# Kernel optimization log

Measured on AMD Instinct MI355X. Metric: run time of the kernel, lower is better.

## Reference

```python
import jax, jax.numpy as jnp
import numpy as np

N_NODES = 100000
N_EDGES = 1600000
IN_CH = 128
HID = 128
N_GRAPHS = 512
N_CLASSES = 64
BN_EPS = 1e-5


def setup_inputs() -> dict:
    key = jax.random.key(0)
    ks = jax.random.split(key, 16)
    x = jax.random.normal(ks[0], (N_NODES, IN_CH), dtype=jnp.float32)
    edge_index = jax.random.randint(ks[1], (2, N_EDGES), 0, N_NODES, dtype=jnp.int32)
    batch = jnp.sort(jax.random.randint(ks[2], (N_NODES,), 0, N_GRAPHS, dtype=jnp.int32))
    def lin(k, fan_in, fan_out):
        s = 1.0 / np.sqrt(fan_in)
        kw, kb = jax.random.split(k)
        W = jax.random.uniform(kw, (fan_in, fan_out), minval=-s, maxval=s, dtype=jnp.float32)
        b = jax.random.uniform(kb, (fan_out,), minval=-s, maxval=s, dtype=jnp.float32)
        return W, b
    W1, b1 = lin(ks[3], IN_CH, HID)
    W2, b2 = lin(ks[4], HID, HID)
    W3, b3 = lin(ks[5], HID, HID)
    Wh, bh = lin(ks[6], HID * 3, N_CLASSES)
    ones = jnp.ones((HID,), jnp.float32)
    zeros = jnp.zeros((HID,), jnp.float32)
    return {
        'x': x, 'edge_index': edge_index, 'batch': batch,
        'W1': W1, 'b1': b1, 'g1': ones, 'be1': zeros,
        'W2': W2, 'b2': b2, 'g2': ones, 'be2': zeros,
        'W3': W3, 'b3': b3, 'g3': ones, 'be3': zeros,
        'Wh': Wh, 'bh': bh,
    }


def _gcn_conv(x, W, b, src, dst, dinv):
    # PyG GCNConv: h = x @ W; out_i = sum_{j->i} dinv_j*dinv_i*h_j + dinv_i^2*h_i (self-loop) + b
    h = x @ W
    coef = (dinv[src] * dinv[dst])[:, None]           # [E,1]
    msg = coef * h[src]                                # [E,H] gather
    agg = jax.ops.segment_sum(msg, dst, num_segments=x.shape[0])  # scatter-add
    return agg + h * (dinv * dinv)[:, None] + b


def _bn(x, g, b):
    mu = jnp.mean(x, axis=0)
    var = jnp.mean((x - mu) ** 2, axis=0)  # biased var (torch training BN)
    return (x - mu) * jax.lax.rsqrt(var + BN_EPS) * g + b


def reference(x, edge_index, batch, W1, b1, g1, be1, W2, b2, g2, be2, W3, b3, g3, be3, Wh, bh):
    src, dst = edge_index[0], edge_index[1]
    n = x.shape[0]
    # degree with self-loops, computed over target nodes (PyG gcn_norm default)
    deg = jax.ops.segment_sum(jnp.ones((src.shape[0],), x.dtype), dst, num_segments=n) + 1.0
    dinv = jax.lax.rsqrt(deg)

    h = jax.nn.relu(_bn(_gcn_conv(x, W1, b1, src, dst, dinv), g1, be1))
    h = jax.nn.relu(_bn(_gcn_conv(h, W2, b2, src, dst, dinv), g2, be2) + h)
    h = jax.nn.relu(_bn(_gcn_conv(h, W3, b3, src, dst, dinv), g3, be3) + h)

    # global mean / add / max pooling per graph
    cnt = jax.ops.segment_sum(jnp.ones((n,), h.dtype), batch, num_segments=N_GRAPHS)
    s = jax.ops.segment_sum(h, batch, num_segments=N_GRAPHS)
    mean = s / jnp.maximum(cnt, 1.0)[:, None]
    mx = jax.ops.segment_max(h, batch, num_segments=N_GRAPHS)
    mx = jnp.where(cnt[:, None] > 0, mx, 0.0)
    pooled = jnp.concatenate([mean, s, mx], axis=1)  # [G, 3H]

    # dropout is identity in eval; single output head
    out = pooled @ Wh + bh
    return out
```

## Files before the change

### kernel.cpp

```cpp
#include <hip/hip_runtime.h>
#include <hip/hip_bf16.h>

#define N_NODES   100000
#define N_EDGES   1600000
#define CH        128
#define N_GRAPHS  512
#define BN_EPS    1e-5f
#define N_PAD     100128

typedef unsigned int uint;
typedef unsigned short ushort_t;

typedef short bf16x8 __attribute__((ext_vector_type(8)));
typedef float f32x4  __attribute__((ext_vector_type(4)));

__device__ __forceinline__ ushort_t f2bf(float f) {
    uint u = __float_as_uint(f);
    uint r = (u + 0x7fffu + ((u >> 16) & 1u)) >> 16;
    return (ushort_t)r;
}
__device__ __forceinline__ float bf2f(ushort_t u) {
    return __uint_as_float(((uint)u) << 16);
}
__device__ __forceinline__ float bf2f_lo(uint u) {
    return __uint_as_float(u << 16);
}
__device__ __forceinline__ float bf2f_hi(uint u) {
    return __uint_as_float(u & 0xffff0000u);
}

#define PREP_W_BLOCKS 128
#define GEMM1_BLOCKS  ((N_NODES + 127) / 128)
#define WLDS_PITCH 136

__global__ __launch_bounds__(256) void k_prep(const int* __restrict__ dst,
                                              int* __restrict__ cnt,
                                              int* __restrict__ rank,
                                              const float* __restrict__ W1,
                                              const float* __restrict__ W2,
                                              const float* __restrict__ W3,
                                              ushort_t* __restrict__ Wt,
                                              const float* __restrict__ x,
                                              ushort_t* __restrict__ H) {
    __shared__ ushort_t lws[128 * WLDS_PITCH];
    const int bid = blockIdx.x;

    if (bid < PREP_W_BLOCKS) {
        int tid = bid * 256 + threadIdx.x;
        int l = tid >> 14;
        int e = tid & 16383;
        int n = e >> 7;
        int k = e & 127;
        const float* W = l ? W3 : W2;
        Wt[l * 16384 + n * 128 + k] = f2bf(W[k * 128 + n]);
        return;
    }

    if (bid < PREP_W_BLOCKS + GEMM1_BLOCKS) {
        const int blk = bid - PREP_W_BLOCKS;
        for (int it = 0; it < 64; ++it) {
            int e = it * 256 + threadIdx.x;
            int k = e >> 7;
            int n = e & 127;
            lws[n * WLDS_PITCH + k] = f2bf(W1[e]);
        }
        __syncthreads();

        const int t = threadIdx.x;
        const int wave = t >> 6;
        const int lane = t & 63;
        const int q = lane >> 4;
        const int r = lane & 15;
        const int row0 = blk * 128 + wave * 32;

        bf16x8 afrag[4][2];
#pragma unroll
        for (int i = 0; i < 2; ++i) {
            int rr = row0 + i * 16 + r;
            if (rr > N_NODES - 1) rr = N_NODES - 1;
            const float* rowp = x + (size_t)rr * 128;
#pragma unroll
            for (int ks = 0; ks < 4; ++ks) {
                const int k0 = ks * 32 + q * 8;
                float4 v0 = *(const float4*)(rowp + k0);
                float4 v1 = *(const float4*)(rowp + k0 + 4);
                bf16x8 av;
                av[0] = (short)f2bf(v0.x); av[1] = (short)f2bf(v0.y);
                av[2] = (short)f2bf(v0.z); av[3] = (short)f2bf(v0.w);
                av[4] = (short)f2bf(v1.x); av[5] = (short)f2bf(v1.y);
                av[6] = (short)f2bf(v1.z); av[7] = (short)f2bf(v1.w);
                afrag[ks][i] = av;
            }
        }

        f32x4 acc[2][8];
#pragma unroll
        for (int i = 0; i < 2; ++i)
#pragma unroll
            for (int j = 0; j < 8; ++j)
                acc[i][j] = (f32x4){0.f, 0.f, 0.f, 0.f};

#pragma unroll
        for (int ks = 0; ks < 4; ++ks) {
            const int k0 = ks * 32 + q * 8;
            bf16x8 b[8];
#pragma unroll
            for (int j = 0; j < 8; ++j)
                b[j] = *(const bf16x8*)&lws[(j * 16 + r) * WLDS_PITCH + k0];
#pragma unroll
            for (int i = 0; i < 2; ++i)
#pragma unroll
                for (int j = 0; j < 8; ++j)
                    acc[i][j] = __builtin_amdgcn_mfma_f32_16x16x32_bf16(afrag[ks][i], b[j], acc[i][j], 0, 0, 0);
        }

#pragma unroll
        for (int i = 0; i < 2; ++i) {
#pragma unroll
            for (int rg = 0; rg < 4; ++rg) {
                int rr = row0 + i * 16 + q * 4 + rg;
                if (rr < N_NODES) {
#pragma unroll
                    for (int j = 0; j < 8; ++j)
                        H[(size_t)rr * 128 + j * 16 + r] = f2bf(acc[i][j][rg]);
                }
            }
        }
        return;
    }

    int e = (bid - PREP_W_BLOCKS - GEMM1_BLOCKS) * 256 + threadIdx.x;
    if (e < N_EDGES) rank[e] = atomicAdd(&cnt[dst[e]], 1);
}

__global__ __launch_bounds__(512) void k_scan1(const int* __restrict__ cnt,
                                               int* __restrict__ lofs,
                                               int* __restrict__ bsum) {
    __shared__ int sd[512];
    int t = threadIdx.x;
    int i = blockIdx.x * 512 + t;
    int v = (i < N_NODES) ? cnt[i] : 0;
    sd[t] = v;
    __syncthreads();
    for (int o = 1; o < 512; o <<= 1) {
        int x = (t >= o) ? sd[t - o] : 0;
        __syncthreads();
        sd[t] += x;
        __syncthreads();
    }
    if (i < N_NODES) lofs[i] = sd[t] - v;
    if (t == 511) bsum[blockIdx.x] = sd[511];
}

__global__ __launch_bounds__(256) void k_scan3(const int* __restrict__ lofs,
                                               const int* __restrict__ bsum,
                                               const int* __restrict__ cnt,
                                               int* __restrict__ offs,
                                               float* __restrict__ dinv,
                                               int nblocks) {
    __shared__ int sd[256];
    int t = threadIdx.x;
    int v = (t < nblocks) ? bsum[t] : 0;
    sd[t] = v;
    __syncthreads();
    for (int o = 1; o < 256; o <<= 1) {
        int x = (t >= o) ? sd[t - o] : 0;
        __syncthreads();
        sd[t] += x;
        __syncthreads();
    }
    int exc = sd[t] - v;
    __syncthreads();
    sd[t] = exc;
    __syncthreads();

    int i = blockIdx.x * 256 + t;
    if (i < N_NODES) {
        offs[i] = lofs[i] + sd[i >> 9];
        dinv[i] = rsqrtf((float)cnt[i] + 1.0f);
    }
    if (i == 0) offs[N_NODES] = N_EDGES;
}

__global__ __launch_bounds__(256) void k_fill(const int* __restrict__ src,
                                              const int* __restrict__ dst,
                                              const int* __restrict__ offs,
                                              const int* __restrict__ rank,
                                              int* __restrict__ csr_src) {
    int e = blockIdx.x * 256 + threadIdx.x;
    if (e >= N_EDGES) return;
    int pos = offs[dst[e]] + rank[e];
    csr_src[pos] = src[e];
}

template<int MODE>
__global__ __launch_bounds__(256) void k_gemm(const ushort_t* __restrict__ Ain,
                                              const ushort_t* __restrict__ Wt,
                                              const float* __restrict__ dinv,
                                              ushort_t* __restrict__ H,
                                              const float* __restrict__ stats,
                                              const float* __restrict__ gamma,
                                              const float* __restrict__ beta,
                                              const ushort_t* __restrict__ RES,
                                              ushort_t* __restrict__ XOUT) {
    const int t = threadIdx.x;
    const int wave = t >> 6;
    const int lane = t & 63;
    const int q = lane >> 4;
    const int r = lane & 15;
    const int row0 = blockIdx.x * 128 + wave * 32;

    bf16x8 afrag[4][2];
    const float invN = 1.0f / (float)N_NODES;

#pragma unroll
    for (int ks = 0; ks < 4; ++ks) {
        const int k0 = ks * 32 + q * 8;
        float sc[8], sh[8];
        {
            float4 sm0 = *(const float4*)&stats[k0];
            float4 sm1 = *(const float4*)&stats[k0 + 4];
            float4 sq0 = *(const float4*)&stats[128 + k0];
            float4 sq1 = *(const float4*)&stats[128 + k0 + 4];
            float4 gm0 = *(const float4*)&gamma[k0];
            float4 gm1 = *(const float4*)&gamma[k0 + 4];
            float4 bt0 = *(const float4*)&beta[k0];
            float4 bt1 = *(const float4*)&beta[k0 + 4];
            float sm[8] = {sm0.x, sm0.y, sm0.z, sm0.w, sm1.x, sm1.y, sm1.z, sm1.w};
            float sq[8] = {sq0.x, sq0.y, sq0.z, sq0.w, sq1.x, sq1.y, sq1.z, sq1.w};
            float gm[8] = {gm0.x, gm0.y, gm0.z, gm0.w, gm1.x, gm1.y, gm1.z, gm1.w};
            float bt[8] = {bt0.x, bt0.y, bt0.z, bt0.w, bt1.x, bt1.y, bt1.z, bt1.w};
#pragma unroll
            for (int u = 0; u < 8; ++u) {
                float mu = sm[u] * invN;
                float s  = gm[u] * rsqrtf(sq[u] * invN - mu * mu + BN_EPS);
                sc[u] = s;
                sh[u] = bt[u] - mu * s;
            }
        }
#pragma unroll
        for (int i = 0; i < 2; ++i) {
            int row = row0 + i * 16 + r;
            int rrc = (row < N_NODES) ? row : (N_NODES - 1);
            uint4 av = *(const uint4*)(Ain + (size_t)rrc * 128 + k0);
            float y[8];
            y[0] = bf2f_lo(av.x); y[1] = bf2f_hi(av.x);
            y[2] = bf2f_lo(av.y); y[3] = bf2f_hi(av.y);
            y[4] = bf2f_lo(av.z); y[5] = bf2f_hi(av.z);
            y[6] = bf2f_lo(av.w); y[7] = bf2f_hi(av.w);
#pragma unroll
            for (int u = 0; u < 8; ++u) y[u] = y[u] * sc[u] + sh[u];
            if constexpr (MODE == 3) {
                uint4 rv = *(const uint4*)(RES + (size_t)rrc * 128 + k0);
                y[0] += bf2f_lo(rv.x); y[1] += bf2f_hi(rv.x);
                y[2] += bf2f_lo(rv.y); y[3] += bf2f_hi(rv.y);
                y[4] += bf2f_lo(rv.z); y[5] += bf2f_hi(rv.z);
                y[6] += bf2f_lo(rv.w); y[7] += bf2f_hi(rv.w);
            }
            uint4 o;
            o.x = (uint)f2bf(fmaxf(y[0], 0.f)) | ((uint)f2bf(fmaxf(y[1], 0.f)) << 16);
            o.y = (uint)f2bf(fmaxf(y[2], 0.f)) | ((uint)f2bf(fmaxf(y[3], 0.f)) << 16);
            o.z = (uint)f2bf(fmaxf(y[4], 0.f)) | ((uint)f2bf(fmaxf(y[5], 0.f)) << 16);
            o.w = (uint)f2bf(fmaxf(y[6], 0.f)) | ((uint)f2bf(fmaxf(y[7], 0.f)) << 16);
            afrag[ks][i] = __builtin_bit_cast(bf16x8, o);
            if (row < N_NODES)
                *(uint4*)(XOUT + (size_t)row * 128 + k0) = o;
        }
    }

    f32x4 acc[2][8];
#pragma unroll
    for (int i = 0; i < 2; ++i)
#pragma unroll
        for (int j = 0; j < 8; ++j)
            acc[i][j] = (f32x4){0.f, 0.f, 0.f, 0.f};

#pragma unroll
    for (int ks = 0; ks < 4; ++ks) {
        const int k0 = ks * 32 + q * 8;
        bf16x8 b[8];
#pragma unroll
        for (int j = 0; j < 8; ++j)
            b[j] = *(const bf16x8*)(Wt + (size_t)(j * 16 + r) * 128 + k0);
#pragma unroll
        for (int i = 0; i < 2; ++i)
#pragma unroll
            for (int j = 0; j < 8; ++j)
                acc[i][j] = __builtin_amdgcn_mfma_f32_16x16x32_bf16(afrag[ks][i], b[j], acc[i][j], 0, 0, 0);
    }

#pragma unroll
    for (int i = 0; i < 2; ++i) {
#pragma unroll
        for (int rg = 0; rg < 4; ++rg) {
            int rr = row0 + i * 16 + q * 4 + rg;
            if (rr < N_NODES) {
                float dv = dinv[rr];
#pragma unroll
                for (int j = 0; j < 8; ++j)
                    H[(size_t)rr * 128 + j * 16 + r] = f2bf(acc[i][j][rg] * dv);
            }
        }
    }
}

template<bool PRESCALED>
__global__ __launch_bounds__(256) void k_gather(const int* __restrict__ csr_src,
                                                const int* __restrict__ offs,
                                                const float* __restrict__ dinv,
                                                const ushort_t* __restrict__ H,
                                                const float* __restrict__ b,
                                                ushort_t* __restrict__ AGG) {
    int node = blockIdx.x * 4 + (threadIdx.x >> 6);
    if (node >= N_NODES) return;
    int lane = threadIdx.x & 63;
    int g = lane >> 4;
    int cl = lane & 15;
    int c = cl * 8;

    float a0 = 0.f, a1 = 0.f, a2 = 0.f, a3 = 0.f;
    float a4 = 0.f, a5 = 0.f, a6 = 0.f, a7 = 0.f;
    float dvn = dinv[node];

#define ACC8(hv)  do { \
        a0 += bf2f_lo((hv).x); a1 += bf2f_hi((hv).x); \
        a2 += bf2f_lo((hv).y); a3 += bf2f_hi((hv).y); \
        a4 += bf2f_lo((hv).z); a5 += bf2f_hi((hv).z); \
        a6 += bf2f_lo((hv).w); a7 += bf2f_hi((hv).w); } while (0)
#define ACC8F(hv, dv)  do { \
        a0 = fmaf((dv), bf2f_lo((hv).x), a0); a1 = fmaf((dv), bf2f_hi((hv).x), a1); \
        a2 = fmaf((dv), bf2f_lo((hv).y), a2); a3 = fmaf((dv), bf2f_hi((hv).y), a3); \
        a4 = fmaf((dv), bf2f_lo((hv).z), a4); a5 = fmaf((dv), bf2f_hi((hv).z), a5); \
        a6 = fmaf((dv), bf2f_lo((hv).w), a6); a7 = fmaf((dv), bf2f_hi((hv).w), a7); } while (0)

    if (g == 0) {
        uint4 hv = *(const uint4*)(H + (size_t)node * 128 + c);
        if constexpr (PRESCALED) { ACC8(hv); } else { ACC8F(hv, dvn); }
    }

    int p = offs[node];
    int end = offs[node + 1];

    for (; p + 16 <= end; p += 16) {
        int s0 = csr_src[p      + g], s1 = csr_src[p +  4 + g];
        int s2 = csr_src[p +  8 + g], s3 = csr_src[p + 12 + g];
        uint4 h0 = *(const uint4*)(H + (size_t)s0 * 128 + c);
        uint4 h1 = *(const uint4*)(H + (size_t)s1 * 128 + c);
        uint4 h2 = *(const uint4*)(H + (size_t)s2 * 128 + c);
        uint4 h3 = *(const uint4*)(H + (size_t)s3 * 128 + c);
        if constexpr (PRESCALED) {
            ACC8(h0); ACC8(h1); ACC8(h2); ACC8(h3);
        } else {
            float d0 = dinv[s0], d1 = dinv[s1], d2 = dinv[s2], d3 = dinv[s3];
            ACC8F(h0, d0); ACC8F(h1, d1); ACC8F(h2, d2); ACC8F(h3, d3);
        }
    }
    for (; p + 4 <= end; p += 4) {
        int s0 = csr_src[p + g];
        uint4 h0 = *(const uint4*)(H + (size_t)s0 * 128 + c);
        if constexpr (PRESCALED) { ACC8(h0); }
        else { float d0 = dinv[s0]; ACC8F(h0, d0); }
    }
    if (p < end) {
        int idx = p + g;
        bool ok = idx < end;
        int s0 = csr_src[ok ? idx : p];
        uint4 h0 = *(const uint4*)(H + (size_t)s0 * 128 + c);
        if constexpr (PRESCALED) { if (ok) ACC8(h0); }
        else { float d0 = dinv[s0]; if (ok) ACC8F(h0, d0); }
    }
#undef ACC8
#undef ACC8F

    a0 += __shfl_xor(a0, 16); a1 += __shfl_xor(a1, 16);
    a2 += __shfl_xor(a2, 16); a3 += __shfl_xor(a3, 16);
    a4 += __shfl_xor(a4, 16); a5 += __shfl_xor(a5, 16);
    a6 += __shfl_xor(a6, 16); a7 += __shfl_xor(a7, 16);
    a0 += __shfl_xor(a0, 32); a1 += __shfl_xor(a1, 32);
    a2 += __shfl_xor(a2, 32); a3 += __shfl_xor(a3, 32);
    a4 += __shfl_xor(a4, 32); a5 += __shfl_xor(a5, 32);
    a6 += __shfl_xor(a6, 32); a7 += __shfl_xor(a7, 32);

    if (g == 0) {
        float4 bv0 = *(const float4*)&b[c];
        float4 bv1 = *(const float4*)&b[c + 4];
        a0 = a0 * dvn + bv0.x; a1 = a1 * dvn + bv0.y;
        a2 = a2 * dvn + bv0.z; a3 = a3 * dvn + bv0.w;
        a4 = a4 * dvn + bv1.x; a5 = a5 * dvn + bv1.y;
        a6 = a6 * dvn + bv1.z; a7 = a7 * dvn + bv1.w;
        uint4 o;
        o.x = (uint)f2bf(a0) | ((uint)f2bf(a1) << 16);
        o.y = (uint)f2bf(a2) | ((uint)f2bf(a3) << 16);
        o.z = (uint)f2bf(a4) | ((uint)f2bf(a5) << 16);
        o.w = (uint)f2bf(a6) | ((uint)f2bf(a7) << 16);
        *(uint4*)(AGG + (size_t)node * 128 + c) = o;
    }
}

__global__ __launch_bounds__(512) void k_bn_stats(const ushort_t* __restrict__ AGG,
                                                  float* __restrict__ stats) {
    __shared__ float red[2][16][128];
    int c4 = (threadIdx.x & 31) * 4;
    int rl = threadIdx.x >> 5;
    float s0 = 0.f, s1 = 0.f, s2 = 0.f, s3 = 0.f;
    float q0 = 0.f, q1 = 0.f, q2 = 0.f, q3 = 0.f;
    for (int i = blockIdx.x * 16 + rl; i < N_NODES; i += gridDim.x * 16) {
        uint2 av = *(const uint2*)&AGG[(size_t)i * 128 + c4];
        float v0 = bf2f_lo(av.x), v1 = bf2f_hi(av.x);
        float v2 = bf2f_lo(av.y), v3 = bf2f_hi(av.y);
        s0 += v0; q0 += v0 * v0;
        s1 += v1; q1 += v1 * v1;
        s2 += v2; q2 += v2 * v2;
        s3 += v3; q3 += v3 * v3;
    }
    red[0][rl][c4 + 0] = s0; red[0][rl][c4 + 1] = s1;
    red[0][rl][c4 + 2] = s2; red[0][rl][c4 + 3] = s3;
    red[1][rl][c4 + 0] = q0; red[1][rl][c4 + 1] = q1;
    red[1][rl][c4 + 2] = q2; red[1][rl][c4 + 3] = q3;
    __syncthreads();
    int t = threadIdx.x;
    if (t < 128) {
        float S = 0.f;
#pragma unroll
        for (int k = 0; k < 16; ++k) S += red[0][k][t];
        atomicAdd(&stats[t], S);
    } else if (t < 256) {
        int c = t - 128;
        float Q = 0.f;
#pragma unroll
        for (int k = 0; k < 16; ++k) Q += red[1][k][c];
        atomicAdd(&stats[128 + c], Q);
    }
}

__global__ __launch_bounds__(512) void k_pool(const ushort_t* __restrict__ AGG,
                                              const ushort_t* __restrict__ RES,
                                              const float* __restrict__ stats,
                                              const float* __restrict__ gamma,
                                              const float* __restrict__ beta,
                                              const int* __restrict__ batch,
                                              float* __restrict__ psum,
                                              float* __restrict__ pmax,
                                              float* __restrict__ pcnt) {
    __shared__ int se[2];
    __shared__ float rs[16][128];
    __shared__ float rm[16][128];
    int g = blockIdx.x;
    if (threadIdx.x < 2) {
        int target = g + (int)threadIdx.x;
        int lo = 0, hi = N_NODES;
        while (lo < hi) {
            int mid = (lo + hi) >> 1;
            if (batch[mid] < target) lo = mid + 1; else hi = mid;
        }
        se[threadIdx.x] = lo;
    }
    __syncthreads();
    int i0 = se[0], i1 = se[1];

    int c4 = (threadIdx.x & 31) * 4;
    int rl = threadIdx.x >> 5;

    const float invN = 1.0f / (float)N_NODES;
    float sc[4], sh[4];
#pragma unroll
    for (int u = 0; u < 4; ++u) {
        float mu = stats[c4 + u] * invN;
        float s = gamma[c4 + u] * rsqrtf(stats[128 + c4 + u] * invN - mu * mu + BN_EPS);
        sc[u] = s;
        sh[u] = beta[c4 + u] - mu * s;
    }

    float s0 = 0.f, s1 = 0.f, s2 = 0.f, s3 = 0.f;
    float m0 = 0.f, m1 = 0.f, m2 = 0.f, m3 = 0.f;
    for (int i = i0 + rl; i < i1; i += 16) {
        uint2 av = *(const uint2*)&AGG[(size_t)i * 128 + c4];
        uint2 rv = *(const uint2*)&RES[(size_t)i * 128 + c4];
        float v0 = fmaxf(bf2f_lo(av.x) * sc[0] + sh[0] + bf2f_lo(rv.x), 0.f);
        float v1 = fmaxf(bf2f_hi(av.x) * sc[1] + sh[1] + bf2f_hi(rv.x), 0.f);
        float v2 = fmaxf(bf2f_lo(av.y) * sc[2] + sh[2] + bf2f_lo(rv.y), 0.f);
        float v3 = fmaxf(bf2f_hi(av.y) * sc[3] + sh[3] + bf2f_hi(rv.y), 0.f);
        s0 += v0; m0 = fmaxf(m0, v0);
        s1 += v1; m1 = fmaxf(m1, v1);
        s2 += v2; m2 = fmaxf(m2, v2);
        s3 += v3; m3 = fmaxf(m3, v3);
    }
    rs[rl][c4 + 0] = s0; rs[rl][c4 + 1] = s1; rs[rl][c4 + 2] = s2; rs[rl][c4 + 3] = s3;
    rm[rl][c4 + 0] = m0; rm[rl][c4 + 1] = m1; rm[rl][c4 + 2] = m2; rm[rl][c4 + 3] = m3;
    __syncthreads();
    int t = threadIdx.x;
    if (t < 128) {
        float S = 0.f, M = 0.f;
#pragma unroll
        for (int k = 0; k < 16; ++k) {
            S += rs[k][t];
            M = fmaxf(M, rm[k][t]);
        }
        psum[g * 128 + t] = S;
        pmax[g * 128 + t] = M;
    }
    if (t == 0) pcnt[g] = (float)(i1 - i0);
}

__global__ __launch_bounds__(64) void k_head(const float* __restrict__ psum,
                                             const float* __restrict__ pmax,
                                             const float* __restrict__ pcnt,
                                             const float* __restrict__ Wh,
                                             const float* __restrict__ bh,
                                             float* __restrict__ out) {
    int g = blockIdx.x;
    int o = threadIdx.x;
    float cnt = pcnt[g];
    float inv = 1.0f / fmaxf(cnt, 1.0f);
    float acc = bh[o];
    for (int c = 0; c < 128; ++c) {
        float s = psum[g * 128 + c];
        float m = pmax[g * 128 + c];
        acc += (s * inv) * Wh[c * 64 + o];
        acc += s * Wh[(128 + c) * 64 + o];
        acc += m * Wh[(256 + c) * 64 + o];
    }
    out[g * 64 + o] = acc;
}

extern "C" void kernel_launch(void* const* d_in, const int* in_sizes, int n_in,
                              void* d_out, int out_size, void* d_ws, size_t ws_size,
                              hipStream_t stream) {
    const float* x     = (const float*)d_in[0];
    const int*   ei    = (const int*)d_in[1];
    const int*   batch = (const int*)d_in[2];
    const float* W1 = (const float*)d_in[3];
    const float* b1 = (const float*)d_in[4];
    const float* g1 = (const float*)d_in[5];
    const float* be1= (const float*)d_in[6];
    const float* W2 = (const float*)d_in[7];
    const float* b2 = (const float*)d_in[8];
    const float* g2 = (const float*)d_in[9];
    const float* be2= (const float*)d_in[10];
    const float* W3 = (const float*)d_in[11];
    const float* b3 = (const float*)d_in[12];
    const float* g3 = (const float*)d_in[13];
    const float* be3= (const float*)d_in[14];
    const float* Wh = (const float*)d_in[15];
    const float* bh = (const float*)d_in[16];

    const int* src = ei;
    const int* dst = ei + N_EDGES;

    char* ws = (char*)d_ws;
    size_t off = 0;

    char* zero_base = ws;
    int*   cnt     = (int*)(ws + off);      off += 400384;
    float* stats   = (float*)(ws + off);    off += 3 * 512 * 4;
    size_t zero_bytes = off;

    float* dinv    = (float*)(ws + off);    off += 512 * 1024;
    ushort_t* XBA  = (ushort_t*)(ws + off); off += (size_t)N_PAD * CH * 2;
    ushort_t* XBB  = (ushort_t*)(ws + off); off += (size_t)N_PAD * CH * 2;
    ushort_t* H    = (ushort_t*)(ws + off); off += (size_t)N_PAD * CH * 2;
    ushort_t* AGG  = (ushort_t*)(ws + off); off += (size_t)N_NODES * CH * 2;
    ushort_t* Wt   = (ushort_t*)(ws + off); off += 2 * 16384 * 2;
    int*   lofs    = (int*)(ws + off);      off += 512 * 1024;
    int*   offs    = (int*)(ws + off);      off += 512 * 1024;
    int*   bsum    = (int*)(ws + off);      off += 4096;
    int*   rank    = (int*)(ws + off);      off += (size_t)N_EDGES * 4;
    int*   csr_src = (int*)(ws + off);      off += (size_t)N_EDGES * 4;
    float* psum    = (float*)(ws + off);    off += (size_t)N_GRAPHS * CH * 4;
    float* pmaxf   = (float*)(ws + off);    off += (size_t)N_GRAPHS * CH * 4;
    float* pcnt    = (float*)(ws + off);    off += 4096;

    const int SCAN_BLOCKS = (N_NODES + 511) / 512;

    hipMemsetAsync(zero_base, 0, zero_bytes, stream);

    const int deg_blocks = (N_EDGES + 255) / 256;
    k_prep<<<PREP_W_BLOCKS + GEMM1_BLOCKS + deg_blocks, 256, 0, stream>>>(
        dst, cnt, rank, W1, W2, W3, Wt, x, H);

    k_scan1<<<SCAN_BLOCKS, 512, 0, stream>>>(cnt, lofs, bsum);
    k_scan3<<<(N_NODES + 255) / 256, 256, 0, stream>>>(lofs, bsum, cnt, offs, dinv, SCAN_BLOCKS);
    k_fill<<<(N_EDGES + 255) / 256, 256, 0, stream>>>(src, dst, offs, rank, csr_src);

    const int gemm_grid   = (N_NODES + 127) / 128;
    const int gather_grid = (N_NODES + 3) / 4;

    float* st1 = stats;
    float* st2 = stats + 512;
    float* st3 = stats + 1024;

    k_gather<false><<<gather_grid, 256, 0, stream>>>(csr_src, offs, dinv, H, b1, AGG);
    k_bn_stats<<<512, 512, 0, stream>>>(AGG, st1);

    k_gemm<2><<<gemm_grid, 256, 0, stream>>>(AGG, Wt, dinv, H,
                                             st1, g1, be1, nullptr, XBB);
    k_gather<true><<<gather_grid, 256, 0, stream>>>(csr_src, offs, dinv, H, b2, AGG);
    k_bn_stats<<<512, 512, 0, stream>>>(AGG, st2);

    k_gemm<3><<<gemm_grid, 256, 0, stream>>>(AGG, Wt + 16384, dinv, H,
                                             st2, g2, be2, XBB, XBA);
    k_gather<true><<<gather_grid, 256, 0, stream>>>(csr_src, offs, dinv, H, b3, AGG);
    k_bn_stats<<<512, 512, 0, stream>>>(AGG, st3);

    k_pool<<<N_GRAPHS, 512, 0, stream>>>(AGG, XBA, st3, g3, be3, batch, psum, pmaxf, pcnt);
    k_head<<<N_GRAPHS, 64, 0, stream>>>(psum, pmaxf, pcnt, Wh, bh, (float*)d_out);
}
```

Before: 574.9 us.

## Halve W1 LDS tile in prep GEMM and fuse head into pool kernel

The first-layer GEMM inside k_prep now stages W1 into shared memory in two 64-column halves, computing half the output columns per pass. This halves LDS use and the accumulator registers, with a min-blocks-per-CU launch bound of 6 to raise occupancy. The cost is a second W1 conversion pass and an extra barrier. Separately, the final linear head is folded into k_pool, which removes one launch and the psum/pmax round trip through global memory.

```diff
diff --git a/kernel.cpp b/kernel.cpp
--- a/kernel.cpp
+++ b/kernel.cpp
@@ -33,16 +33,16 @@
 #define GEMM1_BLOCKS  ((N_NODES + 127) / 128)
 #define WLDS_PITCH 136
 
-__global__ __launch_bounds__(256) void k_prep(const int* __restrict__ dst,
-                                              int* __restrict__ cnt,
-                                              int* __restrict__ rank,
-                                              const float* __restrict__ W1,
-                                              const float* __restrict__ W2,
-                                              const float* __restrict__ W3,
-                                              ushort_t* __restrict__ Wt,
-                                              const float* __restrict__ x,
-                                              ushort_t* __restrict__ H) {
-    __shared__ ushort_t lws[128 * WLDS_PITCH];
+__global__ __launch_bounds__(256, 6) void k_prep(const int* __restrict__ dst,
+                                                 int* __restrict__ cnt,
+                                                 int* __restrict__ rank,
+                                                 const float* __restrict__ W1,
+                                                 const float* __restrict__ W2,
+                                                 const float* __restrict__ W3,
+                                                 ushort_t* __restrict__ Wt,
+                                                 const float* __restrict__ x,
+                                                 ushort_t* __restrict__ H) {
+    __shared__ ushort_t lws[64 * WLDS_PITCH];
     const int bid = blockIdx.x;
 
     if (bid < PREP_W_BLOCKS) {
@@ -58,14 +58,6 @@
 
     if (bid < PREP_W_BLOCKS + GEMM1_BLOCKS) {
         const int blk = bid - PREP_W_BLOCKS;
-        for (int it = 0; it < 64; ++it) {
-            int e = it * 256 + threadIdx.x;
-            int k = e >> 7;
-            int n = e & 127;
-            lws[n * WLDS_PITCH + k] = f2bf(W1[e]);
-        }
-        __syncthreads();
-
         const int t = threadIdx.x;
         const int wave = t >> 6;
         const int lane = t & 63;
@@ -93,36 +85,47 @@
             }
         }
 
-        f32x4 acc[2][8];
-#pragma unroll
-        for (int i = 0; i < 2; ++i)
-#pragma unroll
-            for (int j = 0; j < 8; ++j)
-                acc[i][j] = (f32x4){0.f, 0.f, 0.f, 0.f};
-
-#pragma unroll
-        for (int ks = 0; ks < 4; ++ks) {
-            const int k0 = ks * 32 + q * 8;
-            bf16x8 b[8];
-#pragma unroll
-            for (int j = 0; j < 8; ++j)
-                b[j] = *(const bf16x8*)&lws[(j * 16 + r) * WLDS_PITCH + k0];
+        for (int h = 0; h < 2; ++h) {
+            if (h) __syncthreads();
+            for (int it = 0; it < 32; ++it) {
+                int e = it * 256 + t;
+                int k = e >> 6;
+                int n = e & 63;
+                lws[n * WLDS_PITCH + k] = f2bf(W1[k * 128 + h * 64 + n]);
+            }
+            __syncthreads();
+
+            f32x4 acc[2][4];
 #pragma unroll
             for (int i = 0; i < 2; ++i)
 #pragma unroll
-                for (int j = 0; j < 8; ++j)
-                    acc[i][j] = __builtin_amdgcn_mfma_f32_16x16x32_bf16(afrag[ks][i], b[j], acc[i][j], 0, 0, 0);
-        }
-
-#pragma unroll
-        for (int i = 0; i < 2; ++i) {
-#pragma unroll
-            for (int rg = 0; rg < 4; ++rg) {
-                int rr = row0 + i * 16 + q * 4 + rg;
-                if (rr < N_NODES) {
-#pragma unroll
-                    for (int j = 0; j < 8; ++j)
-                        H[(size_t)rr * 128 + j * 16 + r] = f2bf(acc[i][j][rg]);
+                for (int j = 0; j < 4; ++j)
+                    acc[i][j] = (f32x4){0.f, 0.f, 0.f, 0.f};
+
+#pragma unroll
+            for (int ks = 0; ks < 4; ++ks) {
+                const int k0 = ks * 32 + q * 8;
+                bf16x8 b[4];
+#pragma unroll
+                for (int jj = 0; jj < 4; ++jj)
+                    b[jj] = *(const bf16x8*)&lws[(jj * 16 + r) * WLDS_PITCH + k0];
+#pragma unroll
+                for (int i = 0; i < 2; ++i)
+#pragma unroll
+                    for (int jj = 0; jj < 4; ++jj)
+                        acc[i][jj] = __builtin_amdgcn_mfma_f32_16x16x32_bf16(afrag[ks][i], b[jj], acc[i][jj], 0, 0, 0);
+            }
+
+#pragma unroll
+            for (int i = 0; i < 2; ++i) {
+#pragma unroll
+                for (int rg = 0; rg < 4; ++rg) {
+                    int rr = row0 + i * 16 + q * 4 + rg;
+                    if (rr < N_NODES) {
+#pragma unroll
+                        for (int jj = 0; jj < 4; ++jj)
+                            H[(size_t)rr * 128 + h * 64 + jj * 16 + r] = f2bf(acc[i][jj][rg]);
+                    }
                 }
             }
         }
@@ -439,12 +442,13 @@
                                               const float* __restrict__ gamma,
                                               const float* __restrict__ beta,
                                               const int* __restrict__ batch,
-                                              float* __restrict__ psum,
-                                              float* __restrict__ pmax,
-                                              float* __restrict__ pcnt) {
+                                              const float* __restrict__ Wh,
+                                              const float* __restrict__ bh,
+                                              float* __restrict__ out) {
     __shared__ int se[2];
     __shared__ float rs[16][128];
     __shared__ float rm[16][128];
+    __shared__ float hp[8][64];
     int g = blockIdx.x;
     if (threadIdx.x < 2) {
         int target = g + (int)threadIdx.x;
@@ -496,31 +500,32 @@
             S += rs[k][t];
             M = fmaxf(M, rm[k][t]);
         }
-        psum[g * 128 + t] = S;
-        pmax[g * 128 + t] = M;
-    }
-    if (t == 0) pcnt[g] = (float)(i1 - i0);
-}
-
-__global__ __launch_bounds__(64) void k_head(const float* __restrict__ psum,
-                                             const float* __restrict__ pmax,
-                                             const float* __restrict__ pcnt,
-                                             const float* __restrict__ Wh,
-                                             const float* __restrict__ bh,
-                                             float* __restrict__ out) {
-    int g = blockIdx.x;
-    int o = threadIdx.x;
-    float cnt = pcnt[g];
-    float inv = 1.0f / fmaxf(cnt, 1.0f);
-    float acc = bh[o];
-    for (int c = 0; c < 128; ++c) {
-        float s = psum[g * 128 + c];
-        float m = pmax[g * 128 + c];
-        acc += (s * inv) * Wh[c * 64 + o];
-        acc += s * Wh[(128 + c) * 64 + o];
-        acc += m * Wh[(256 + c) * 64 + o];
-    }
-    out[g * 64 + o] = acc;
+        rs[0][t] = S;
+        rm[0][t] = M;
+    }
+    __syncthreads();
+
+    float inv = 1.0f / fmaxf((float)(i1 - i0), 1.0f);
+    int o = t & 63;
+    int kc = t >> 6;
+    float acc = 0.f;
+#pragma unroll
+    for (int u = 0; u < 16; ++u) {
+        int c = kc * 16 + u;
+        float S = rs[0][c];
+        float M = rm[0][c];
+        acc += (S * inv) * Wh[c * 64 + o];
+        acc += S * Wh[(128 + c) * 64 + o];
+        acc += M * Wh[(256 + c) * 64 + o];
+    }
+    hp[kc][o] = acc;
+    __syncthreads();
+    if (t < 64) {
+        float r = bh[t];
+#pragma unroll
+        for (int k = 0; k < 8; ++k) r += hp[k][t];
+        out[g * 64 + t] = r;
+    }
 }
 
 extern "C" void kernel_launch(void* const* d_in, const int* in_sizes, int n_in,
@@ -566,9 +571,6 @@
     int*   bsum    = (int*)(ws + off);      off += 4096;
     int*   rank    = (int*)(ws + off);      off += (size_t)N_EDGES * 4;
     int*   csr_src = (int*)(ws + off);      off += (size_t)N_EDGES * 4;
-    float* psum    = (float*)(ws + off);    off += (size_t)N_GRAPHS * CH * 4;
-    float* pmaxf   = (float*)(ws + off);    off += (size_t)N_GRAPHS * CH * 4;
-    float* pcnt    = (float*)(ws + off);    off += 4096;
 
     const int SCAN_BLOCKS = (N_NODES + 511) / 512;
 
@@ -602,6 +604,5 @@
     k_gather<true><<<gather_grid, 256, 0, stream>>>(csr_src, offs, dinv, H, b3, AGG);
     k_bn_stats<<<512, 512, 0, stream>>>(AGG, st3);
 
-    k_pool<<<N_GRAPHS, 512, 0, stream>>>(AGG, XBA, st3, g3, be3, batch, psum, pmaxf, pcnt);
-    k_head<<<N_GRAPHS, 64, 0, stream>>>(psum, pmaxf, pcnt, Wh, bh, (float*)d_out);
-}
+    k_pool<<<N_GRAPHS, 512, 0, stream>>>(AGG, XBA, st3, g3, be3, batch, Wh, bh, (float*)d_out);
+}
```

After: 627.7 us. 1.09x slower.
